# Performance work log

Measured on AMD Instinct MI355X. Metric: run time of the kernel, lower is better.

## Reference

```python
import jax, jax.numpy as jnp
import numpy as np

N_NODES = 100000
N_EDGES = 1600000
IN_FEATS = 256
OUT_FEATS = 128


def setup_inputs() -> dict:
    key = jax.random.key(0)
    k1, k2, k3, k4 = jax.random.split(key, 4)
    feat = jax.random.normal(k1, (N_NODES, IN_FEATS), dtype=jnp.float32)
    W = jax.random.normal(k2, (IN_FEATS, OUT_FEATS), dtype=jnp.float32)
    src = jax.random.randint(k3, (N_EDGES,), 0, N_NODES, dtype=jnp.int64)
    dst = jax.random.randint(k4, (N_EDGES,), 0, N_NODES, dtype=jnp.int64)
    return {"feat": feat, "W": W, "src": src, "dst": dst}


def reference(feat, W, src, dst):
    # h_self = feat @ W  -> [N, out_feats]
    h_self = feat @ W
    # update_all(copy_src('h','m'), sum('m','neigh')): gather source features,
    # scatter-sum at destination nodes (SpMM over the edge list).
    msgs = h_self[src]                                        # [E, out_feats]
    h_neigh = jax.ops.segment_sum(msgs, dst, num_segments=N_NODES)
    # in-degree per node
    degs = jax.ops.segment_sum(jnp.ones(dst.shape, jnp.float32), dst,
                               num_segments=N_NODES)          # [N]
    rst = (h_neigh + h_self) / (degs[:, None] + 1.0)
    return jax.nn.relu(rst)
```

## Files before the change

kernel.cpp:

```cpp
#include <hip/hip_runtime.h>
#include <hip/hip_bf16.h>


#define IN_FEATS 256
#define OUT_FEATS 128
#define NUM_NODES 100000
#define NUM_EDGES 1600000

#define NB 782
#define EC 128
#define CHUNK_E 12500
#define BCAP 3072
#define GEMM_BLOCKS 391

typedef __attribute__((ext_vector_type(8))) short short8;
typedef __attribute__((ext_vector_type(8))) unsigned short ushort8;
typedef __attribute__((ext_vector_type(4))) float f32x4;

static __device__ inline unsigned short f2bfu(float x) {
    union { __hip_bfloat16 h; unsigned short u; } c;
    c.h = __float2bfloat16(x);
    return c.u;
}
static __device__ inline ushort2 f2bfu2(float x, float y) {
    union { __hip_bfloat162 h; ushort2 u; } c;
    c.h = __float22bfloat162_rn(make_float2(x, y));
    return c.u;
}
static __device__ inline float bf2f(unsigned short h) {
    return __uint_as_float((unsigned)h << 16);
}

__global__ __launch_bounds__(256) void convert_hist(
    const float* __restrict__ W, unsigned short* __restrict__ Wt,
    const int* __restrict__ dst, int* __restrict__ counts)
{
    int b = blockIdx.x;
    int t = threadIdx.x;
    if (b < 128) {
        int i = b * 256 + t;
        int n = i >> 8;
        int k = i & 255;
        Wt[i] = f2bfu(W[(size_t)k * OUT_FEATS + n]);
        return;
    }
    int c = b - 128;
    __shared__ int hist[NB];
    for (int i = t; i < NB; i += 256) hist[i] = 0;
    __syncthreads();
    const int4* dp = (const int4*)(dst + c * CHUNK_E);
    for (int i = t; i < CHUNK_E / 4; i += 256) {
        int4 d4 = dp[i];
        atomicAdd(&hist[d4.x >> 7], 1);
        atomicAdd(&hist[d4.y >> 7], 1);
        atomicAdd(&hist[d4.z >> 7], 1);
        atomicAdd(&hist[d4.w >> 7], 1);
    }
    __syncthreads();
    for (int i = t; i < NB; i += 256) counts[c * NB + i] = hist[i];
}

__global__ __launch_bounds__(128) void scan_chunks(
    int* __restrict__ counts, int* __restrict__ bucket_total)
{
    __shared__ int sd[128];
    int b = blockIdx.x, t = threadIdx.x;
    int v = counts[t * NB + b];
    sd[t] = v;
    __syncthreads();
    for (int o = 1; o < 128; o <<= 1) {
        int x = (t >= o) ? sd[t - o] : 0;
        __syncthreads();
        sd[t] += x;
        __syncthreads();
    }
    counts[t * NB + b] = sd[t] - v;
    if (t == 127) bucket_total[b] = sd[127];
}

__global__ __launch_bounds__(256) void scan_buckets(
    const int* __restrict__ bucket_total, int* __restrict__ bucket_base)
{
    __shared__ int sd[256];
    int t = threadIdx.x;
    int base = t * 4;
    int v0 = 0, v1 = 0, v2 = 0, v3 = 0;
    if (base + 3 < NB) {
        int4 v = *(const int4*)&bucket_total[base];
        v0 = v.x; v1 = v.y; v2 = v.z; v3 = v.w;
    } else {
        if (base + 0 < NB) v0 = bucket_total[base + 0];
        if (base + 1 < NB) v1 = bucket_total[base + 1];
        if (base + 2 < NB) v2 = bucket_total[base + 2];
        if (base + 3 < NB) v3 = bucket_total[base + 3];
    }
    int s = v0 + v1 + v2 + v3;
    sd[t] = s;
    __syncthreads();
    for (int o = 1; o < 256; o <<= 1) {
        int x = (t >= o) ? sd[t - o] : 0;
        __syncthreads();
        sd[t] += x;
        __syncthreads();
    }
    int e0 = sd[t] - s, e1 = e0 + v0, e2 = e1 + v1, e3 = e2 + v2;
    if (base + 0 < NB) bucket_base[base + 0] = e0;
    if (base + 1 < NB) bucket_base[base + 1] = e1;
    if (base + 2 < NB) bucket_base[base + 2] = e2;
    if (base + 3 < NB) bucket_base[base + 3] = e3;
}

__global__ __launch_bounds__(512, 4) void gemm_scatter(
    const float* __restrict__ feat, const unsigned short* __restrict__ Wt,
    unsigned short* __restrict__ hself16, int M,
    const int* __restrict__ src, const int* __restrict__ dst,
    const int* __restrict__ counts, const int* __restrict__ bucket_base,
    int* __restrict__ bedges)
{
    __shared__ char smem_raw[65536];
    const int tid = threadIdx.x;

    if (blockIdx.x >= GEMM_BLOCKS) {
        int c = blockIdx.x - GEMM_BLOCKS;
        int* cur = (int*)smem_raw;
        for (int i = tid; i < NB; i += 512)
            cur[i] = bucket_base[i] + counts[c * NB + i];
        __syncthreads();
        const int4* dp = (const int4*)(dst + c * CHUNK_E);
        const int4* sp = (const int4*)(src + c * CHUNK_E);
        for (int i = tid; i < CHUNK_E / 4; i += 512) {
            int4 d4 = dp[i];
            int4 s4 = sp[i];
            int dv[4] = { d4.x, d4.y, d4.z, d4.w };
            int sv[4] = { s4.x, s4.y, s4.z, s4.w };
#pragma unroll
            for (int j = 0; j < 4; ++j) {
                int d = dv[j];
                int slot = atomicAdd(&cur[d >> 7], 1);
                bedges[slot] = sv[j] | ((d & 127) << 17);
            }
        }
        return;
    }

    unsigned short* Bl = (unsigned short*)smem_raw;

    {
        int n = tid >> 2;
        int gbase = (tid & 3) * 8;
#pragma unroll
        for (int j = 0; j < 8; ++j) {
            int g = gbase + j;
            ushort8 v = *(const ushort8*)(Wt + (size_t)n * IN_FEATS + g * 8);
            *(ushort8*)(Bl + n * IN_FEATS + ((g ^ (n & 7)) * 8)) = v;
        }
    }
    __syncthreads();

    const int w  = tid >> 6;
    const int l  = tid & 63;
    const int lf = l & 15;
    const int lg = (l >> 4) & 3;
    const int bm0 = blockIdx.x * 256;
    const int rbase = bm0 + w * 32;

    f32x4 acc[2][8];
#pragma unroll
    for (int mt = 0; mt < 2; ++mt)
#pragma unroll
        for (int nt = 0; nt < 8; ++nt)
            acc[mt][nt] = (f32x4){0.f, 0.f, 0.f, 0.f};

#pragma unroll 2
    for (int k0 = 0; k0 < IN_FEATS; k0 += 32) {
        int k8 = k0 >> 3;
        short8 af[2];
#pragma unroll
        for (int mt = 0; mt < 2; ++mt) {
            int grow = rbase + mt * 16 + lf;
            if (grow < M) {
                const float4* ap = (const float4*)(feat + (size_t)grow * IN_FEATS + k0 + lg * 8);
                float4 f0 = ap[0];
                float4 f1 = ap[1];
                ushort2 c0 = f2bfu2(f0.x, f0.y);
                ushort2 c1 = f2bfu2(f0.z, f0.w);
                ushort2 c2 = f2bfu2(f1.x, f1.y);
                ushort2 c3 = f2bfu2(f1.z, f1.w);
                af[mt] = (short8){ (short)c0.x, (short)c0.y, (short)c1.x, (short)c1.y,
                                   (short)c2.x, (short)c2.y, (short)c3.x, (short)c3.y };
            } else {
                af[mt] = (short8){ 0, 0, 0, 0, 0, 0, 0, 0 };
            }
        }
#pragma unroll
        for (int nh = 0; nh < 2; ++nh) {
            short8 bf[4];
#pragma unroll
            for (int q = 0; q < 4; ++q) {
                int nt = nh * 4 + q;
                int n = nt * 16 + lf;
                int g = (k8 + lg) ^ (lf & 7);
                bf[q] = *(const short8*)(Bl + n * IN_FEATS + g * 8);
            }
#pragma unroll
            for (int q = 0; q < 4; ++q) {
                int nt = nh * 4 + q;
                acc[0][nt] = __builtin_amdgcn_mfma_f32_16x16x32_bf16(af[0], bf[q], acc[0][nt], 0, 0, 0);
                acc[1][nt] = __builtin_amdgcn_mfma_f32_16x16x32_bf16(af[1], bf[q], acc[1][nt], 0, 0, 0);
            }
        }
    }

    __syncthreads();
    unsigned short* ep = (unsigned short*)smem_raw;
#pragma unroll
    for (int mt = 0; mt < 2; ++mt)
#pragma unroll
        for (int nt = 0; nt < 8; ++nt)
#pragma unroll
            for (int r = 0; r < 4; ++r) {
                int row = w * 32 + mt * 16 + lg * 4 + r;
                ep[row * 128 + nt * 16 + lf] = f2bfu(acc[mt][nt][r]);
            }
    __syncthreads();
#pragma unroll
    for (int i = 0; i < 8; ++i) {
        int lrow = w * 32 + i * 4 + (l >> 4);
        ushort8 v = *(const ushort8*)(ep + lrow * 128 + (l & 15) * 8);
        int grow = bm0 + lrow;
        if (grow < M)
            *(ushort8*)(hself16 + (size_t)grow * OUT_FEATS + (l & 15) * 8) = v;
    }
}

__global__ __launch_bounds__(512, 8) void sort_gather(
    const int* __restrict__ bucket_base, const int* __restrict__ bucket_total,
    const int* __restrict__ bedges, const unsigned short* __restrict__ hself16,
    float* __restrict__ out)
{
    __shared__ int sorted[BCAP];
    __shared__ int cnt[128], off[128], cursor[128], sd[128];

    int b = blockIdx.x, t = threadIdx.x;
    int base = bucket_base[b];
    int tot = bucket_total[b];
    if (tot > BCAP) tot = BCAP;
    int nnodes = NUM_NODES - b * 128;
    if (nnodes > 128) nnodes = 128;

    if (t < 128) cnt[t] = 0;
    __syncthreads();
    for (int i = t; i < tot; i += 512)
        atomicAdd(&cnt[bedges[base + i] >> 17], 1);
    __syncthreads();
    if (t < 128) sd[t] = cnt[t];
    __syncthreads();
    for (int o = 1; o < 128; o <<= 1) {
        int x = 0;
        if (t < 128 && t >= o) x = sd[t - o];
        __syncthreads();
        if (t < 128) sd[t] += x;
        __syncthreads();
    }
    if (t < 128) { int e = sd[t] - cnt[t]; off[t] = e; cursor[t] = e; }
    __syncthreads();
    for (int i = t; i < tot; i += 512) {
        int e = bedges[base + i];
        int r = atomicAdd(&cursor[e >> 17], 1);
        sorted[r] = e & 0x1FFFF;
    }
    __syncthreads();

    int w = t >> 6, l = t & 63, lg = l >> 4, lf = l & 15;
    for (int ln = w; ln < nnodes; ln += 8) {
        int beg = off[ln];
        int end = beg + cnt[ln];
        float acc[8];
#pragma unroll
        for (int i = 0; i < 8; ++i) acc[i] = 0.f;
        for (int j0 = beg; j0 < end; j0 += 16) {
            int  jj[4];
            bool pp[4];
            int  ss[4];
#pragma unroll
            for (int q = 0; q < 4; ++q) {
                jj[q] = j0 + q * 4 + lg;
                pp[q] = jj[q] < end;
                ss[q] = pp[q] ? sorted[jj[q]] : 0;
            }
            ushort8 h[4];
#pragma unroll
            for (int q = 0; q < 4; ++q)
                h[q] = *(const ushort8*)(hself16 + (size_t)ss[q] * OUT_FEATS + lf * 8);
#pragma unroll
            for (int q = 0; q < 4; ++q)
                if (pp[q]) {
#pragma unroll
                    for (int i = 0; i < 8; ++i) acc[i] += bf2f(h[q][i]);
                }
        }
#pragma unroll
        for (int i = 0; i < 8; ++i) {
            acc[i] += __shfl_xor(acc[i], 16, 64);
            acc[i] += __shfl_xor(acc[i], 32, 64);
        }
        if (lg == 0) {
            int n = b * 128 + ln;
            float inv = 1.0f / (float)(end - beg + 1);
            ushort8 hs = *(const ushort8*)(hself16 + (size_t)n * OUT_FEATS + lf * 8);
            float v[8];
#pragma unroll
            for (int i = 0; i < 8; ++i)
                v[i] = fmaxf((acc[i] + bf2f(hs[i])) * inv, 0.f);
            float4* op = (float4*)(out + (size_t)n * OUT_FEATS + lf * 8);
            op[0] = make_float4(v[0], v[1], v[2], v[3]);
            op[1] = make_float4(v[4], v[5], v[6], v[7]);
        }
    }
}

extern "C" void kernel_launch(void* const* d_in, const int* in_sizes, int n_in,
                              void* d_out, int out_size, void* d_ws, size_t ws_size,
                              hipStream_t stream) {
    const float* feat = (const float*)d_in[0];
    const float* W    = (const float*)d_in[1];
    const int*   src  = (const int*)d_in[2];
    const int*   dst  = (const int*)d_in[3];
    float* out = (float*)d_out;

    char* ws = (char*)d_ws;
    unsigned short* hself16 = (unsigned short*)ws;
    unsigned short* Wt      = (unsigned short*)(ws + 25600000);
    int* counts       = (int*)(ws + 25665536);
    int* bucket_total = (int*)(ws + 26065920);
    int* bucket_base  = (int*)(ws + 26069120);
    int* bedges       = (int*)(ws + 26072320);

    convert_hist<<<256, 256, 0, stream>>>(W, Wt, dst, counts);
    scan_chunks<<<NB, 128, 0, stream>>>(counts, bucket_total);
    scan_buckets<<<1, 256, 0, stream>>>(bucket_total, bucket_base);
    gemm_scatter<<<GEMM_BLOCKS + EC, 512, 0, stream>>>(
        feat, Wt, hself16, NUM_NODES, src, dst, counts, bucket_base, bedges);
    sort_gather<<<NB, 512, 0, stream>>>(bucket_base, bucket_total, bedges, hself16, out);
}
```

Measured before the change: 285.3 us.

## Fuse histogram and scans via last-block pattern and global atomic cursors

Replaces the per-chunk count matrix and two scan kernels with a single kernel. Block histograms are accumulated into a global histogram with atomics, and the last block to finish scans it into bucket bases. The scatter blocks now recompute their local histogram and reserve slots in each bucket with global atomicAdd on a cursor. This removes two kernel launches and the 128x782 count matrix traffic, at the cost of a second pass over dst, a memset, and an edge order within each bucket that is no longer deterministic.

```diff
diff --git a/kernel.cpp b/kernel.cpp
--- a/kernel.cpp
+++ b/kernel.cpp
@@ -31,102 +31,96 @@
     return __uint_as_float((unsigned)h << 16);
 }
 
-__global__ __launch_bounds__(256) void convert_hist(
+__global__ __launch_bounds__(256) void hist_convert_scan(
     const float* __restrict__ W, unsigned short* __restrict__ Wt,
-    const int* __restrict__ dst, int* __restrict__ counts)
+    const int* __restrict__ dst, int* __restrict__ hist, int* __restrict__ done,
+    int* __restrict__ bucket_base, int* __restrict__ bucket_total,
+    int* __restrict__ gcursor)
 {
-    int b = blockIdx.x;
-    int t = threadIdx.x;
+    __shared__ int lh[NB];
+    __shared__ int sd[256];
+    __shared__ int last_flag;
+    int b = blockIdx.x, t = threadIdx.x;
+
     if (b < 128) {
-        int i = b * 256 + t;
+        for (int i = t; i < NB; i += 256) lh[i] = 0;
+        __syncthreads();
+        const int4* dp = (const int4*)(dst + b * CHUNK_E);
+        for (int i = t; i < CHUNK_E / 4; i += 256) {
+            int4 d4 = dp[i];
+            atomicAdd(&lh[d4.x >> 7], 1);
+            atomicAdd(&lh[d4.y >> 7], 1);
+            atomicAdd(&lh[d4.z >> 7], 1);
+            atomicAdd(&lh[d4.w >> 7], 1);
+        }
+        __syncthreads();
+        for (int i = t; i < NB; i += 256) {
+            int h = lh[i];
+            if (h) atomicAdd(&hist[i], h);
+        }
+    } else {
+        int i = (b - 128) * 256 + t;
         int n = i >> 8;
         int k = i & 255;
         Wt[i] = f2bfu(W[(size_t)k * OUT_FEATS + n]);
-        return;
-    }
-    int c = b - 128;
-    __shared__ int hist[NB];
-    for (int i = t; i < NB; i += 256) hist[i] = 0;
-    __syncthreads();
-    const int4* dp = (const int4*)(dst + c * CHUNK_E);
-    for (int i = t; i < CHUNK_E / 4; i += 256) {
-        int4 d4 = dp[i];
-        atomicAdd(&hist[d4.x >> 7], 1);
-        atomicAdd(&hist[d4.y >> 7], 1);
-        atomicAdd(&hist[d4.z >> 7], 1);
-        atomicAdd(&hist[d4.w >> 7], 1);
-    }
-    __syncthreads();
-    for (int i = t; i < NB; i += 256) counts[c * NB + i] = hist[i];
-}
-
-__global__ __launch_bounds__(128) void scan_chunks(
-    int* __restrict__ counts, int* __restrict__ bucket_total)
-{
-    __shared__ int sd[128];
-    int b = blockIdx.x, t = threadIdx.x;
-    int v = counts[t * NB + b];
-    sd[t] = v;
-    __syncthreads();
-    for (int o = 1; o < 128; o <<= 1) {
-        int x = (t >= o) ? sd[t - o] : 0;
-        __syncthreads();
-        sd[t] += x;
-        __syncthreads();
-    }
-    counts[t * NB + b] = sd[t] - v;
-    if (t == 127) bucket_total[b] = sd[127];
-}
-
-__global__ __launch_bounds__(256) void scan_buckets(
-    const int* __restrict__ bucket_total, int* __restrict__ bucket_base)
-{
-    __shared__ int sd[256];
-    int t = threadIdx.x;
-    int base = t * 4;
-    int v0 = 0, v1 = 0, v2 = 0, v3 = 0;
-    if (base + 3 < NB) {
-        int4 v = *(const int4*)&bucket_total[base];
-        v0 = v.x; v1 = v.y; v2 = v.z; v3 = v.w;
-    } else {
-        if (base + 0 < NB) v0 = bucket_total[base + 0];
-        if (base + 1 < NB) v1 = bucket_total[base + 1];
-        if (base + 2 < NB) v2 = bucket_total[base + 2];
-        if (base + 3 < NB) v3 = bucket_total[base + 3];
-    }
-    int s = v0 + v1 + v2 + v3;
-    sd[t] = s;
-    __syncthreads();
-    for (int o = 1; o < 256; o <<= 1) {
-        int x = (t >= o) ? sd[t - o] : 0;
-        __syncthreads();
-        sd[t] += x;
-        __syncthreads();
-    }
-    int e0 = sd[t] - s, e1 = e0 + v0, e2 = e1 + v1, e3 = e2 + v2;
-    if (base + 0 < NB) bucket_base[base + 0] = e0;
-    if (base + 1 < NB) bucket_base[base + 1] = e1;
-    if (base + 2 < NB) bucket_base[base + 2] = e2;
-    if (base + 3 < NB) bucket_base[base + 3] = e3;
+    }
+
+    __threadfence();
+    __syncthreads();
+    if (t == 0) last_flag = (atomicAdd(done, 1) == 255);
+    __syncthreads();
+    if (last_flag) {
+        int base = t * 4;
+        int v0 = 0, v1 = 0, v2 = 0, v3 = 0;
+        if (base + 0 < NB) v0 = atomicAdd(&hist[base + 0], 0);
+        if (base + 1 < NB) v1 = atomicAdd(&hist[base + 1], 0);
+        if (base + 2 < NB) v2 = atomicAdd(&hist[base + 2], 0);
+        if (base + 3 < NB) v3 = atomicAdd(&hist[base + 3], 0);
+        int s = v0 + v1 + v2 + v3;
+        sd[t] = s;
+        __syncthreads();
+        for (int o = 1; o < 256; o <<= 1) {
+            int x = (t >= o) ? sd[t - o] : 0;
+            __syncthreads();
+            sd[t] += x;
+            __syncthreads();
+        }
+        int e0 = sd[t] - s, e1 = e0 + v0, e2 = e1 + v1, e3 = e2 + v2;
+        if (base + 0 < NB) { bucket_base[base + 0] = e0; bucket_total[base + 0] = v0; gcursor[base + 0] = e0; }
+        if (base + 1 < NB) { bucket_base[base + 1] = e1; bucket_total[base + 1] = v1; gcursor[base + 1] = e1; }
+        if (base + 2 < NB) { bucket_base[base + 2] = e2; bucket_total[base + 2] = v2; gcursor[base + 2] = e2; }
+        if (base + 3 < NB) { bucket_base[base + 3] = e3; bucket_total[base + 3] = v3; gcursor[base + 3] = e3; }
+    }
 }
 
 __global__ __launch_bounds__(512, 4) void gemm_scatter(
     const float* __restrict__ feat, const unsigned short* __restrict__ Wt,
     unsigned short* __restrict__ hself16, int M,
     const int* __restrict__ src, const int* __restrict__ dst,
-    const int* __restrict__ counts, const int* __restrict__ bucket_base,
-    int* __restrict__ bedges)
+    int* __restrict__ gcursor, int* __restrict__ bedges)
 {
     __shared__ char smem_raw[65536];
     const int tid = threadIdx.x;
 
     if (blockIdx.x >= GEMM_BLOCKS) {
         int c = blockIdx.x - GEMM_BLOCKS;
-        int* cur = (int*)smem_raw;
-        for (int i = tid; i < NB; i += 512)
-            cur[i] = bucket_base[i] + counts[c * NB + i];
+        int* lh = (int*)smem_raw;
+        for (int i = tid; i < NB; i += 512) lh[i] = 0;
         __syncthreads();
         const int4* dp = (const int4*)(dst + c * CHUNK_E);
+        for (int i = tid; i < CHUNK_E / 4; i += 512) {
+            int4 d4 = dp[i];
+            atomicAdd(&lh[d4.x >> 7], 1);
+            atomicAdd(&lh[d4.y >> 7], 1);
+            atomicAdd(&lh[d4.z >> 7], 1);
+            atomicAdd(&lh[d4.w >> 7], 1);
+        }
+        __syncthreads();
+        for (int i = tid; i < NB; i += 512) {
+            int h = lh[i];
+            lh[i] = h ? atomicAdd(&gcursor[i], h) : 0;
+        }
+        __syncthreads();
         const int4* sp = (const int4*)(src + c * CHUNK_E);
         for (int i = tid; i < CHUNK_E / 4; i += 512) {
             int4 d4 = dp[i];
@@ -134,17 +128,16 @@
             int dv[4] = { d4.x, d4.y, d4.z, d4.w };
             int sv[4] = { s4.x, s4.y, s4.z, s4.w };
 #pragma unroll
-            for (int j = 0; j < 4; ++j) {
-                int d = dv[j];
-                int slot = atomicAdd(&cur[d >> 7], 1);
-                bedges[slot] = sv[j] | ((d & 127) << 17);
+            for (int q = 0; q < 4; ++q) {
+                int d = dv[q];
+                int slot = atomicAdd(&lh[d >> 7], 1);
+                bedges[slot] = sv[q] | ((d & 127) << 17);
             }
         }
         return;
     }
 
     unsigned short* Bl = (unsigned short*)smem_raw;
-
     {
         int n = tid >> 2;
         int gbase = (tid & 3) * 8;
@@ -331,15 +324,20 @@
     char* ws = (char*)d_ws;
     unsigned short* hself16 = (unsigned short*)ws;
     unsigned short* Wt      = (unsigned short*)(ws + 25600000);
-    int* counts       = (int*)(ws + 25665536);
-    int* bucket_total = (int*)(ws + 26065920);
-    int* bucket_base  = (int*)(ws + 26069120);
-    int* bedges       = (int*)(ws + 26072320);
-
-    convert_hist<<<256, 256, 0, stream>>>(W, Wt, dst, counts);
-    scan_chunks<<<NB, 128, 0, stream>>>(counts, bucket_total);
-    scan_buckets<<<1, 256, 0, stream>>>(bucket_total, bucket_base);
+    int* hist         = (int*)(ws + 25665536);
+    int* done         = (int*)(ws + 25668664);
+    int* bucket_base  = (int*)(ws + 25668672);
+    int* bucket_total = (int*)(ws + 25671808);
+    int* gcursor      = (int*)(ws + 25674944);
+    int* bedges       = (int*)(ws + 25678080);
+
+    hipMemsetAsync(hist, 0, 3132, stream);
+
+    hist_convert_scan<<<256, 256, 0, stream>>>(
+        W, Wt, dst, hist, done, bucket_base, bucket_total, gcursor);
+
     gemm_scatter<<<GEMM_BLOCKS + EC, 512, 0, stream>>>(
-        feat, Wt, hself16, NUM_NODES, src, dst, counts, bucket_base, bedges);
+        feat, Wt, hself16, NUM_NODES, src, dst, gcursor, bedges);
+
     sort_gather<<<NB, 512, 0, stream>>>(bucket_base, bucket_total, bedges, hself16, out);
 }
```

After: 305.7 us. 7.1% more time.
